# Kernel optimization log

Hardware: AMD Instinct MI355X
Metric: run time of the kernel (lower is better)

The kernel has to match this reference:

```python
import jax, jax.numpy as jnp
import numpy as np

T, B, C, HF, H, W, E, TOP_K = 4, 32, 384, 1536, 14, 14, 8, 2
AUX_W = 0.01
ALPHA = 2.0  # spikingjelly ATan surrogate default

@jax.custom_vjp
def spike(v):
    return (v >= 0.0).astype(v.dtype)

def _spike_fwd(v):
    return spike(v), v

def _spike_bwd(v, g):
    sg = (ALPHA / 2.0) / (1.0 + (jnp.pi / 2.0 * ALPHA * v) ** 2)
    return (g * sg,)

spike.defvjp(_spike_fwd, _spike_bwd)

def lif_multistep(x, tau):
    # x: (T, ...). decay_input=True, v_threshold=1, hard reset to 0, detach_reset
    def step(v, xt):
        v = v + (xt - v) / tau
        s = spike(v - 1.0)
        v = v * (1.0 - jax.lax.stop_gradient(s))
        return v, s
    _, s = jax.lax.scan(step, jnp.zeros_like(x[0]), x)
    return s

def bn_eval(y, gamma, beta, mean, var, eps=1e-5):
    inv = gamma / jnp.sqrt(var + eps)
    return y * inv[None, :, None, None] + (beta - mean * inv)[None, :, None, None]

def setup_inputs() -> dict:
    key = jax.random.key(0)
    ks = jax.random.split(key, 8)
    d = {"x": jax.random.normal(ks[0], (T, B, C, H, W), jnp.float32)}
    d["rw"] = jax.random.normal(ks[1], (E, C), jnp.float32) * 0.02
    d["rb"] = jnp.zeros((E,), jnp.float32)
    d["r_gamma"] = jnp.ones((E,), jnp.float32)
    d["r_beta"] = jnp.zeros((E,), jnp.float32)
    d["r_mean"] = jax.random.normal(ks[2], (E,), jnp.float32) * 0.01
    d["r_var"] = jax.random.uniform(ks[3], (E,), jnp.float32, 0.75, 1.25)
    d["w1"] = jax.random.normal(ks[4], (E, HF, C), jnp.float32) * 0.02
    d["b1"] = jnp.zeros((E, HF), jnp.float32)
    d["g1"] = jnp.ones((E, HF), jnp.float32)
    d["be1"] = jnp.zeros((E, HF), jnp.float32)
    d["m1"] = jax.random.normal(ks[5], (E, HF), jnp.float32) * 0.01
    d["v1"] = jnp.ones((E, HF), jnp.float32)
    d["w2"] = jax.random.normal(ks[6], (E, C, HF), jnp.float32) * 0.02
    d["b2"] = jnp.zeros((E, C), jnp.float32)
    d["g2"] = jnp.ones((E, C), jnp.float32)
    d["be2"] = jnp.zeros((E, C), jnp.float32)
    d["m2"] = jax.random.normal(ks[7], (E, C), jnp.float32) * 0.01
    d["v2"] = jnp.ones((E, C), jnp.float32)
    d["taus"] = jnp.linspace(1.5, 4.0, E, dtype=jnp.float32)
    return d

def reference(x, rw, rb, r_gamma, r_beta, r_mean, r_var,
              w1, b1, g1, be1, m1, v1, w2, b2, g2, be2, m2, v2, taus):
    Tn, Bn, Cn, Hn, Wn = x.shape
    N = Tn * Bn
    # ---- SpikeRouter ----
    s = lif_multistep(x, 2.0)                                   # (T,B,C,H,W)
    r = jnp.einsum('tbchw,ec->tbehw', s, rw) + rb[None, None, :, None, None]
    r = bn_eval(r.reshape(N, E, Hn, Wn), r_gamma, r_beta, r_mean, r_var)
    logits = r.mean(axis=(-2, -1))                              # (N,E)
    probs = jax.nn.softmax(logits, axis=-1)
    tkw, tki = jax.lax.top_k(probs, TOP_K)
    tkw = tkw / tkw.sum(axis=-1, keepdims=True)
    one_hot = jax.nn.one_hot(tki, E, dtype=x.dtype)             # (N,K,E)
    gate = (one_hot * tkw[..., None]).sum(axis=1)               # (N,E), 0 for unselected
    # ---- expert dispatch/combine (dense, math-equivalent: gate==0 masks out) ----
    xt = x.reshape(N, Cn, Hn, Wn)
    out = jnp.zeros_like(xt)
    for e in range(E):
        s1 = spike(xt / taus[e] - 1.0)                          # T=1 LIF step
        h = jnp.einsum('nchw,oc->nohw', s1, w1[e]) + b1[e][None, :, None, None]
        h = bn_eval(h, g1[e], be1[e], m1[e], v1[e])
        s2 = spike(h / taus[e] - 1.0)
        o = jnp.einsum('nchw,oc->nohw', s2, w2[e]) + b2[e][None, :, None, None]
        o = bn_eval(o, g2[e], be2[e], m2[e], v2[e])
        o = o + xt                                              # final residual
        out = out + gate[:, e, None, None, None] * o
    # ---- Switch-style load balancing loss ----
    f = one_hot.sum(axis=1).mean(axis=0)                        # fraction routed per expert
    p = probs.mean(axis=0)
    aux = AUX_W * E * jnp.sum(f * p)
    return out.reshape(Tn, Bn, Cn, Hn, Wn), aux
```

## Files before the change

kernel.cpp:

```cpp
#include <hip/hip_runtime.h>
#include <hip/hip_bf16.h>
#include <cstdint>
#include <math.h>

#define T_  4
#define B_  32
#define C_  384
#define HF_ 1536
#define HW_ 196
#define E_  8
#define N_  128
#define NROW 1792
#define NGT  50176
#define LCAP 64

#define LIFW (B_ * C_ / 4)
#define TRB  (E_ * 12 * 24)
#define PRB  48
#define COMBB ((N_ * C_ * 49) / 256)

__global__ __launch_bounds__(256) void k_lifprep(
    const float* __restrict__ x, float* __restrict__ cnt,
    unsigned int* __restrict__ levels4,
    const float* __restrict__ w1, __hip_bfloat16* __restrict__ w1t,
    const float* b1, const float* g1, const float* be1,
    const float* m1, const float* v1,
    const float* b2, const float* g2, const float* be2,
    const float* m2, const float* v2,
    const float* taus,
    float* A, float* Bc, float* const2, float* inv2v,
    float* rowmaxp, int* header) {
  __shared__ float tile[64][33];
  int blk = blockIdx.x;
  int tid = threadIdx.x;

  if (blk < LIFW) {
    int lane = tid & 63, wave = tid >> 6;
    int bc = blk * 4 + wave;
    bool act = lane < 49;
    float te[E_];
    #pragma unroll
    for (int e2 = 0; e2 < E_; ++e2) {
      float t = taus[e2];
      float y = t;
      #pragma unroll
      for (int it = 0; it < 4; ++it) {
        float cnd = __uint_as_float(__float_as_uint(y) - 1u);
        if (cnd / t - 1.0f >= 0.0f) y = cnd; else break;
      }
      te[e2] = y;
    }
    const float4* xr = (const float4*)x;
    size_t rb = (size_t)bc * 49 + (act ? lane : 0);
    const size_t ts4 = (size_t)B_ * C_ * 49;
    float4 v = {0.f, 0.f, 0.f, 0.f};
    unsigned int counts = 0;
    unsigned int pk[T_];
    #pragma unroll
    for (int t = 0; t < T_; ++t) {
      float4 xv;
      if (act) xv = xr[rb + (size_t)t * ts4];
      else { xv.x = xv.y = xv.z = xv.w = -1e30f; }
      int l0 = 0, l1 = 0, l2 = 0, l3 = 0;
      #pragma unroll
      for (int e2 = 0; e2 < E_; ++e2) {
        l0 += (xv.x >= te[e2]) ? 1 : 0;
        l1 += (xv.y >= te[e2]) ? 1 : 0;
        l2 += (xv.z >= te[e2]) ? 1 : 0;
        l3 += (xv.w >= te[e2]) ? 1 : 0;
      }
      pk[t] = (unsigned int)l0 | ((unsigned int)l1 << 8) |
              ((unsigned int)l2 << 16) | ((unsigned int)l3 << 24);
      v.x = v.x + (xv.x - v.x) * 0.5f;
      v.y = v.y + (xv.y - v.y) * 0.5f;
      v.z = v.z + (xv.z - v.z) * 0.5f;
      v.w = v.w + (xv.w - v.w) * 0.5f;
      int cl = 0;
      if (v.x - 1.0f >= 0.0f) { v.x = 0.f; ++cl; }
      if (v.y - 1.0f >= 0.0f) { v.y = 0.f; ++cl; }
      if (v.z - 1.0f >= 0.0f) { v.z = 0.f; ++cl; }
      if (v.w - 1.0f >= 0.0f) { v.w = 0.f; ++cl; }
      counts += (unsigned int)cl << (8 * t);
    }
    if (act) {
      #pragma unroll
      for (int t = 0; t < T_; ++t)
        levels4[rb + (size_t)t * ts4] = pk[t];
    }
    #pragma unroll
    for (int off = 1; off < 64; off <<= 1)
      counts += (unsigned int)__shfl_xor((int)counts, off, 64);
    if (lane == 0) {
      #pragma unroll
      for (int t = 0; t < T_; ++t)
        cnt[(size_t)t * B_ * C_ + bc] = (float)((counts >> (8 * t)) & 0xffu);
    }
  } else if (blk < LIFW + TRB) {
    int rem = blk - LIFW;
    int e = rem / 288, r2 = rem % 288;
    int ct = r2 / 24, ot = r2 % 24;
    int c0 = ct * 32, o0 = ot * 64;
    int cl = tid & 31, olb = tid >> 5;
    #pragma unroll
    for (int it = 0; it < 8; ++it) {
      int ol = olb + it * 8;
      tile[ol][cl] = w1[(size_t)(e * HF_ + o0 + ol) * C_ + c0 + cl];
    }
    __syncthreads();
    int ol2 = tid & 63, clb = tid >> 6;
    #pragma unroll
    for (int it = 0; it < 8; ++it) {
      int cl2 = clb + it * 4;
      w1t[(size_t)(e * C_ + c0 + cl2) * HF_ + o0 + ol2] =
          __float2bfloat16(tile[ol2][cl2]);
    }
    if (tid < 32) {
      float m = 0.f;
      for (int ol = 0; ol < 64; ++ol) {
        float bv = __bfloat162float(__float2bfloat16(tile[ol][tid]));
        m = fmaxf(m, fabsf(bv));
      }
      rowmaxp[(size_t)(e * C_ + c0 + tid) * 24 + ot] = m;
    }
  } else {
    int idx = (blk - LIFW - TRB) * 256 + tid;
    if (idx < 64) header[idx] = 0;
    if (idx < E_ * HF_) {
      int e = idx / HF_;
      float inv = g1[idx] / sqrtf(v1[idx] + 1e-5f);
      float sh  = be1[idx] - m1[idx] * inv;
      A[idx]  = inv;
      Bc[idx] = inv * b1[idx] + sh - taus[e];
    }
    if (idx < E_ * C_) {
      float inv = g2[idx] / sqrtf(v2[idx] + 1e-5f);
      const2[idx] = b2[idx] * inv + (be2[idx] - m2[idx] * inv);
      inv2v[idx]  = inv;
    }
  }
}

__global__ __launch_bounds__(256) void k_router(
    const float* __restrict__ cnt, const float* __restrict__ rw,
    const float* rb, const float* rg, const float* rbeta,
    const float* rmean, const float* rvar,
    const float* __restrict__ const2,
    const float* __restrict__ rowmaxp, float* __restrict__ rowmax,
    const float* __restrict__ A, const float* __restrict__ Bc,
    float* __restrict__ thrmin,
    int* sel_e, float* sel_g, float* gsum, float* K,
    float* f_acc, float* p_acc) {
  __shared__ float sc[C_ + 256 + E_];
  __shared__ int s_i1, s_i2;
  __shared__ float s_g1, s_g2;
  int bid = blockIdx.x, tid = threadIdx.x;

  if (bid < N_) {
    int n = bid;
    float* part = sc + C_;
    float* lg = part + 256;
    for (int c = tid; c < C_; c += 256) sc[c] = cnt[(size_t)n * C_ + c];
    __syncthreads();
    {
      int e = tid >> 5, sub = tid & 31;
      float d = 0.f;
      for (int c = sub; c < C_; c += 32) d += rw[e * C_ + c] * sc[c];
      part[tid] = d;
    }
    __syncthreads();
    if (tid < E_) {
      float dot = 0.f;
      #pragma unroll
      for (int j = 0; j < 32; ++j) dot += part[tid * 32 + j];
      float inv = rg[tid] / sqrtf(rvar[tid] + 1e-5f);
      lg[tid] = (dot * (1.0f / HW_) + rb[tid]) * inv +
                (rbeta[tid] - rmean[tid] * inv);
    }
    __syncthreads();
    if (tid == 0) {
      float m = lg[0];
      for (int e = 1; e < E_; ++e) m = fmaxf(m, lg[e]);
      float pr[E_]; float s = 0.f;
      for (int e = 0; e < E_; ++e) { pr[e] = expf(lg[e] - m); s += pr[e]; }
      float invs = 1.0f / s;
      for (int e = 0; e < E_; ++e) pr[e] *= invs;
      int i1 = 0;
      for (int e = 1; e < E_; ++e) if (pr[e] > pr[i1]) i1 = e;
      int i2 = (i1 == 0) ? 1 : 0;
      for (int e = 0; e < E_; ++e) if (e != i1 && pr[e] > pr[i2]) i2 = e;
      float w = pr[i1] + pr[i2];
      float ga = pr[i1] / w, gb = pr[i2] / w;
      sel_e[2 * n] = i1; sel_e[2 * n + 1] = i2;
      sel_g[2 * n] = ga; sel_g[2 * n + 1] = gb;
      gsum[n] = ga + gb;
      s_i1 = i1; s_i2 = i2; s_g1 = ga; s_g2 = gb;
      atomicAdd(&f_acc[i1], 1.0f);
      atomicAdd(&f_acc[i2], 1.0f);
      for (int e = 0; e < E_; ++e) atomicAdd(&p_acc[e], pr[e]);
    }
    __syncthreads();
    int i1 = s_i1, i2 = s_i2; float ga = s_g1, gb = s_g2;
    for (int c = tid; c < C_; c += 256)
      K[(size_t)n * C_ + c] =
          ga * const2[i1 * C_ + c] + gb * const2[i2 * C_ + c];
  } else if (bid < N_ + 12) {
    int idx = (bid - N_) * 256 + tid;
    if (idx < E_ * C_) {
      float m = 0.f;
      #pragma unroll
      for (int t = 0; t < 24; ++t) m = fmaxf(m, rowmaxp[(size_t)idx * 24 + t]);
      rowmax[idx] = m;
    }
  } else {
    float* red = sc;
    for (int e = 0; e < E_; ++e) {
      float m = INFINITY;
      for (int o = tid; o < HF_; o += 256) {
        float a = A[e * HF_ + o], b = Bc[e * HF_ + o];
        float thr = (a != 0.0f) ? (-b / fabsf(a))
                                : ((b >= 0.0f) ? -INFINITY : INFINITY);
        m = fminf(m, thr);
      }
      red[tid] = m;
      __syncthreads();
      for (int s = 128; s > 0; s >>= 1) {
        if (tid < s) red[tid] = fminf(red[tid], red[tid + s]);
        __syncthreads();
      }
      if (tid == 0) thrmin[e] = red[0];
      __syncthreads();
    }
  }
}

__global__ __launch_bounds__(256) void k_lists(
    const float* __restrict__ x, const unsigned char* __restrict__ levels,
    const int* __restrict__ sel_e,
    const float* __restrict__ rowmax, const float* __restrict__ thrmin,
    unsigned short* __restrict__ list16,
    int* __restrict__ queue, int* __restrict__ qcount,
    const float* __restrict__ f_acc, const float* __restrict__ p_acc,
    float* __restrict__ aux_out,
    const float* __restrict__ gsum, const float* __restrict__ K,
    float* __restrict__ out) {
  __shared__ unsigned char xs8[14 * C_];
  int bid = blockIdx.x, tid = threadIdx.x;

  if (bid >= NROW) {
    int idx = (bid - NROW) * 256 + tid;
    int nc = idx / 49;
    float g = gsum[nc / C_];
    float kc = K[nc];
    float4 v = ((const float4*)x)[idx];
    v.x = g * v.x + kc;
    v.y = g * v.y + kc;
    v.z = g * v.z + kc;
    v.w = g * v.w + kc;
    ((float4*)out)[idx] = v;
    return;
  }

  int lane = tid & 63, wave = tid >> 6;
  int n = bid / 14, h = bid - n * 14;
  unsigned long long lmask = (1ull << lane) - 1ull;

  if (bid == 0 && tid == 0) {
    float s = 0.f;
    for (int e = 0; e < E_; ++e)
      s += (f_acc[e] * (1.0f / N_)) * (p_acc[e] * (1.0f / N_));
    *aux_out = 0.01f * E_ * s;
  }

  for (int c = tid; c < C_; c += 256) {
    const unsigned short* p =
        (const unsigned short*)(levels + (size_t)(n * C_ + c) * HW_ + h * 14);
    #pragma unroll
    for (int i = 0; i < 7; ++i) {
      unsigned short u = p[i];
      xs8[(2 * i) * C_ + c]     = (unsigned char)(u & 0xff);
      xs8[(2 * i + 1) * C_ + c] = (unsigned char)(u >> 8);
    }
  }
  __syncthreads();

  for (int t = wave; t < 28; t += 4) {
    int k = t / 14, w = t - k * 14;
    int pair = 2 * n + k;
    int e = sel_e[pair];
    const float* rme = rowmax + e * C_;
    unsigned long long masks[6];
    int nnz = 0;
    float myb = 0.f;
    #pragma unroll
    for (int cb = 0; cb < 6; ++cb) {
      int c = cb * 64 + lane;
      bool sp = ((int)xs8[w * C_ + c] > e);
      unsigned long long m = __ballot(sp);
      masks[cb] = m;
      if (sp) myb += rme[c];
      nnz += __popcll(m);
    }
    #pragma unroll
    for (int off = 1; off < 64; off <<= 1) myb += __shfl_xor(myb, off, 64);
    bool prune = (myb < thrmin[e] - 1e-4f);
    if (!prune) {
      int tw = pair * 196 + h * 14 + w;
      size_t lbase = (size_t)tw * LCAP;
      int cum = 0;
      #pragma unroll
      for (int cb = 0; cb < 6; ++cb) {
        unsigned long long m = masks[cb];
        bool sp = (m >> lane) & 1ull;
        int pos = cum + __popcll(m & lmask);
        if (sp && pos < LCAP) list16[lbase + pos] = (unsigned short)(cb * 64 + lane);
        cum += __popcll(m);
      }
      if (lane == 0) {
        int nv = nnz < LCAP ? nnz : LCAP;
        int qi = atomicAdd(qcount, 1);
        queue[qi] = tw | (nv << 20);
      }
    }
  }
}

__global__ __launch_bounds__(256, 4) void k_gather(
    const __hip_bfloat16* __restrict__ w1t,
    const float* __restrict__ A, const float* __restrict__ Bc,
    const int* __restrict__ sel_e, const float* __restrict__ sel_g,
    const int* __restrict__ queue, const int* __restrict__ qcount,
    const unsigned short* __restrict__ list16,
    const float* __restrict__ inv2v, const float* __restrict__ w2,
    float* __restrict__ out) {
  int nq = *qcount;
  int wid = blockIdx.x * 4 + (threadIdx.x >> 6);
  int lane = threadIdx.x & 63;
  int nwaves = gridDim.x * 4;

  for (int qi = wid; qi < nq; qi += nwaves) {
    int ent = queue[qi];
    int tw = ent & 0xFFFFF;
    int nnz = ent >> 20;
    int pair = tw / HW_, pos = tw - pair * HW_;
    int n = pair >> 1;
    int e = sel_e[pair];
    int lv = (int)list16[(size_t)tw * LCAP + lane];
    const uint4* wb = (const uint4*)(w1t + (size_t)e * C_ * HF_);

    #pragma unroll
    for (int pass = 0; pass < 3; ++pass) {
      const uint4* wbp = wb + pass * 64 + lane;
      float acc[8];
      #pragma unroll
      for (int q = 0; q < 8; ++q) acc[q] = 0.f;
      int j = 0;
      for (; j + 4 <= nnz; j += 4) {
        int c0 = __shfl(lv, j + 0);
        int c1 = __shfl(lv, j + 1);
        int c2 = __shfl(lv, j + 2);
        int c3 = __shfl(lv, j + 3);
        uint4 a = wbp[c0 * 192];
        uint4 b = wbp[c1 * 192];
        uint4 c = wbp[c2 * 192];
        uint4 d = wbp[c3 * 192];
        uint32_t ua[4] = {a.x, a.y, a.z, a.w};
        uint32_t ub[4] = {b.x, b.y, b.z, b.w};
        uint32_t uc[4] = {c.x, c.y, c.z, c.w};
        uint32_t ud[4] = {d.x, d.y, d.z, d.w};
        #pragma unroll
        for (int q = 0; q < 4; ++q) {
          acc[2 * q]     += __uint_as_float(ua[q] << 16) + __uint_as_float(ub[q] << 16) +
                            __uint_as_float(uc[q] << 16) + __uint_as_float(ud[q] << 16);
          acc[2 * q + 1] += __uint_as_float(ua[q] & 0xffff0000u) + __uint_as_float(ub[q] & 0xffff0000u) +
                            __uint_as_float(uc[q] & 0xffff0000u) + __uint_as_float(ud[q] & 0xffff0000u);
        }
      }
      for (; j < nnz; ++j) {
        int c0 = __shfl(lv, j);
        uint4 a = wbp[c0 * 192];
        uint32_t ua[4] = {a.x, a.y, a.z, a.w};
        #pragma unroll
        for (int q = 0; q < 4; ++q) {
          acc[2 * q]     += __uint_as_float(ua[q] << 16);
          acc[2 * q + 1] += __uint_as_float(ua[q] & 0xffff0000u);
        }
      }
      int k2 = (pass * 64 + lane) * 2;
      float4 Av0 = ((const float4*)(A + e * HF_))[k2];
      float4 Av1 = ((const float4*)(A + e * HF_))[k2 + 1];
      float4 Bv0 = ((const float4*)(Bc + e * HF_))[k2];
      float4 Bv1 = ((const float4*)(Bc + e * HF_))[k2 + 1];
      float av[8] = {Av0.x, Av0.y, Av0.z, Av0.w, Av1.x, Av1.y, Av1.z, Av1.w};
      float bv[8] = {Bv0.x, Bv0.y, Bv0.z, Bv0.w, Bv1.x, Bv1.y, Bv1.z, Bv1.w};
      #pragma unroll
      for (int q = 0; q < 8; ++q) {
        unsigned long long fm = __ballot(av[q] * acc[q] + bv[q] >= 0.0f);
        while (fm) {
          int b = __ffsll((unsigned long long)fm) - 1;
          fm &= fm - 1;
          int o = (pass * 64 + b) * 8 + q;
          float gk = sel_g[pair];
          const float* w2r = w2 + (size_t)e * C_ * HF_ + o;
          const float* ivr = inv2v + e * C_;
          for (int c = lane; c < C_; c += 64) {
            atomicAdd(&out[((size_t)(n * C_ + c)) * HW_ + pos],
                      gk * ivr[c] * w2r[(size_t)c * HF_]);
          }
        }
      }
    }
  }
}

extern "C" void kernel_launch(void* const* d_in, const int* in_sizes, int n_in,
                              void* d_out, int out_size, void* d_ws, size_t ws_size,
                              hipStream_t stream) {
  const float* x       = (const float*)d_in[0];
  const float* rw      = (const float*)d_in[1];
  const float* rb      = (const float*)d_in[2];
  const float* r_gamma = (const float*)d_in[3];
  const float* r_beta  = (const float*)d_in[4];
  const float* r_mean  = (const float*)d_in[5];
  const float* r_var   = (const float*)d_in[6];
  const float* w1      = (const float*)d_in[7];
  const float* b1      = (const float*)d_in[8];
  const float* g1      = (const float*)d_in[9];
  const float* be1     = (const float*)d_in[10];
  const float* m1      = (const float*)d_in[11];
  const float* v1      = (const float*)d_in[12];
  const float* w2      = (const float*)d_in[13];
  const float* b2      = (const float*)d_in[14];
  const float* g2      = (const float*)d_in[15];
  const float* be2     = (const float*)d_in[16];
  const float* m2      = (const float*)d_in[17];
  const float* v2      = (const float*)d_in[18];
  const float* taus    = (const float*)d_in[19];
  float* out = (float*)d_out;

  char* ws = (char*)d_ws;
  int*   header = (int*)ws;
  float* f_acc  = (float*)ws + 8;
  float* p_acc  = (float*)ws + 16;
  float* cnt    = (float*)(ws + 256);
  int*   sel_e  = (int*)(ws + 196864);
  float* sel_g  = (float*)(ws + 197888);
  float* gsum   = (float*)(ws + 198912);
  float* K      = (float*)(ws + 199424);
  float* A      = (float*)(ws + 396032);
  float* Bc     = (float*)(ws + 445184);
  float* const2 = (float*)(ws + 494336);
  float* inv2v  = (float*)(ws + 506624);
  __hip_bfloat16* w1t = (__hip_bfloat16*)(ws + 715520);
  int*   queue  = (int*)(ws + 10152704);
  unsigned short* list16 = (unsigned short*)(ws + 10353408);
  float* rowmaxp = (float*)(ws + 16775936);
  float* rowmax  = (float*)(ws + 17070848);
  float* thrmin  = (float*)(ws + 17083136);
  unsigned char* levels = (unsigned char*)(ws + 17084416);
  int* qcount = header + 1;

  k_lifprep<<<LIFW + TRB + PRB, 256, 0, stream>>>(
      x, cnt, (unsigned int*)levels, w1, w1t,
      b1, g1, be1, m1, v1, b2, g2, be2, m2, v2, taus,
      A, Bc, const2, inv2v, rowmaxp, header);
  k_router<<<N_ + 13, 256, 0, stream>>>(
      cnt, rw, rb, r_gamma, r_beta, r_mean, r_var, const2,
      rowmaxp, rowmax, A, Bc, thrmin,
      sel_e, sel_g, gsum, K, f_acc, p_acc);
  k_lists<<<NROW + COMBB, 256, 0, stream>>>(
      x, levels, sel_e, rowmax, thrmin, list16, queue, qcount,
      f_acc, p_acc, out + (out_size - 1), gsum, K, out);
  k_gather<<<2048, 256, 0, stream>>>(
      w1t, A, Bc, sel_e, sel_g, queue, qcount, list16, inv2v, w2, out);
}
```

Measured before the change: 201.4 us.

## Prune hidden-unit groups in gather via per-group weight-max upper bounds

```diff
diff --git a/kernel.cpp b/kernel.cpp
--- a/kernel.cpp
+++ b/kernel.cpp
@@ -13,6 +13,7 @@
 #define NROW 1792
 #define NGT  50176
 #define LCAP 64
+#define NGRP 24
 
 #define LIFW (B_ * C_ / 4)
 #define TRB  (E_ * 12 * 24)
@@ -120,7 +121,7 @@
         float bv = __bfloat162float(__float2bfloat16(tile[ol][tid]));
         m = fmaxf(m, fabsf(bv));
       }
-      rowmaxp[(size_t)(e * C_ + c0 + tid) * 24 + ot] = m;
+      rowmaxp[(size_t)(e * C_ + c0 + tid) * NGRP + ot] = m;
     }
   } else {
     int idx = (blk - LIFW - TRB) * 256 + tid;
@@ -147,7 +148,7 @@
     const float* __restrict__ const2,
     const float* __restrict__ rowmaxp, float* __restrict__ rowmax,
     const float* __restrict__ A, const float* __restrict__ Bc,
-    float* __restrict__ thrmin,
+    float* __restrict__ thrmin, float* __restrict__ thrg,
     int* sel_e, float* sel_g, float* gsum, float* K,
     float* f_acc, float* p_acc) {
   __shared__ float sc[C_ + 256 + E_];
@@ -208,27 +209,29 @@
     if (idx < E_ * C_) {
       float m = 0.f;
       #pragma unroll
-      for (int t = 0; t < 24; ++t) m = fmaxf(m, rowmaxp[(size_t)idx * 24 + t]);
+      for (int t = 0; t < NGRP; ++t)
+        m = fmaxf(m, rowmaxp[(size_t)idx * NGRP + t]);
       rowmax[idx] = m;
     }
   } else {
-    float* red = sc;
+    int lane = tid & 63, wv = tid >> 6;
     for (int e = 0; e < E_; ++e) {
-      float m = INFINITY;
-      for (int o = tid; o < HF_; o += 256) {
+      for (int g = wv; g < NGRP; g += 4) {
+        int o = g * 64 + lane;
         float a = A[e * HF_ + o], b = Bc[e * HF_ + o];
         float thr = (a != 0.0f) ? (-b / fabsf(a))
                                 : ((b >= 0.0f) ? -INFINITY : INFINITY);
-        m = fminf(m, thr);
-      }
-      red[tid] = m;
-      __syncthreads();
-      for (int s = 128; s > 0; s >>= 1) {
-        if (tid < s) red[tid] = fminf(red[tid], red[tid + s]);
-        __syncthreads();
-      }
-      if (tid == 0) thrmin[e] = red[0];
-      __syncthreads();
+        #pragma unroll
+        for (int off = 1; off < 64; off <<= 1)
+          thr = fminf(thr, __shfl_xor(thr, off, 64));
+        if (lane == 0) thrg[e * NGRP + g] = thr;
+      }
+    }
+    __syncthreads();
+    if (tid < E_) {
+      float m = INFINITY;
+      for (int g = 0; g < NGRP; ++g) m = fminf(m, thrg[tid * NGRP + g]);
+      thrmin[tid] = m;
     }
   }
 }
@@ -330,6 +333,7 @@
     const int* __restrict__ sel_e, const float* __restrict__ sel_g,
     const int* __restrict__ queue, const int* __restrict__ qcount,
     const unsigned short* __restrict__ list16,
+    const float* __restrict__ grpmax, const float* __restrict__ thrg,
     const float* __restrict__ inv2v, const float* __restrict__ w2,
     float* __restrict__ out) {
   int nq = *qcount;
@@ -345,67 +349,61 @@
     int n = pair >> 1;
     int e = sel_e[pair];
     int lv = (int)list16[(size_t)tw * LCAP + lane];
-    const uint4* wb = (const uint4*)(w1t + (size_t)e * C_ * HF_);
-
-    #pragma unroll
-    for (int pass = 0; pass < 3; ++pass) {
-      const uint4* wbp = wb + pass * 64 + lane;
-      float acc[8];
-      #pragma unroll
-      for (int q = 0; q < 8; ++q) acc[q] = 0.f;
-      int j = 0;
-      for (; j + 4 <= nnz; j += 4) {
-        int c0 = __shfl(lv, j + 0);
-        int c1 = __shfl(lv, j + 1);
-        int c2 = __shfl(lv, j + 2);
-        int c3 = __shfl(lv, j + 3);
-        uint4 a = wbp[c0 * 192];
-        uint4 b = wbp[c1 * 192];
-        uint4 c = wbp[c2 * 192];
-        uint4 d = wbp[c3 * 192];
-        uint32_t ua[4] = {a.x, a.y, a.z, a.w};
-        uint32_t ub[4] = {b.x, b.y, b.z, b.w};
-        uint32_t uc[4] = {c.x, c.y, c.z, c.w};
-        uint32_t ud[4] = {d.x, d.y, d.z, d.w};
-        #pragma unroll
-        for (int q = 0; q < 4; ++q) {
-          acc[2 * q]     += __uint_as_float(ua[q] << 16) + __uint_as_float(ub[q] << 16) +
-                            __uint_as_float(uc[q] << 16) + __uint_as_float(ud[q] << 16);
-          acc[2 * q + 1] += __uint_as_float(ua[q] & 0xffff0000u) + __uint_as_float(ub[q] & 0xffff0000u) +
-                            __uint_as_float(uc[q] & 0xffff0000u) + __uint_as_float(ud[q] & 0xffff0000u);
-        }
-      }
-      for (; j < nnz; ++j) {
-        int c0 = __shfl(lv, j);
-        uint4 a = wbp[c0 * 192];
-        uint32_t ua[4] = {a.x, a.y, a.z, a.w};
-        #pragma unroll
-        for (int q = 0; q < 4; ++q) {
-          acc[2 * q]     += __uint_as_float(ua[q] << 16);
-          acc[2 * q + 1] += __uint_as_float(ua[q] & 0xffff0000u);
-        }
-      }
-      int k2 = (pass * 64 + lane) * 2;
-      float4 Av0 = ((const float4*)(A + e * HF_))[k2];
-      float4 Av1 = ((const float4*)(A + e * HF_))[k2 + 1];
-      float4 Bv0 = ((const float4*)(Bc + e * HF_))[k2];
-      float4 Bv1 = ((const float4*)(Bc + e * HF_))[k2 + 1];
-      float av[8] = {Av0.x, Av0.y, Av0.z, Av0.w, Av1.x, Av1.y, Av1.z, Av1.w};
-      float bv[8] = {Bv0.x, Bv0.y, Bv0.z, Bv0.w, Bv1.x, Bv1.y, Bv1.z, Bv1.w};
-      #pragma unroll
-      for (int q = 0; q < 8; ++q) {
-        unsigned long long fm = __ballot(av[q] * acc[q] + bv[q] >= 0.0f);
-        while (fm) {
-          int b = __ffsll((unsigned long long)fm) - 1;
-          fm &= fm - 1;
-          int o = (pass * 64 + b) * 8 + q;
-          float gk = sel_g[pair];
-          const float* w2r = w2 + (size_t)e * C_ * HF_ + o;
-          const float* ivr = inv2v + e * C_;
-          for (int c = lane; c < C_; c += 64) {
-            atomicAdd(&out[((size_t)(n * C_ + c)) * HW_ + pos],
-                      gk * ivr[c] * w2r[(size_t)c * HF_]);
-          }
+
+    bool actg = lane < NGRP;
+    int gl = actg ? lane : 0;
+    const float* gme = grpmax + (size_t)e * C_ * NGRP;
+    float myb = 0.f;
+    int j = 0;
+    for (; j + 4 <= nnz; j += 4) {
+      int c0 = __shfl(lv, j + 0), c1 = __shfl(lv, j + 1);
+      int c2 = __shfl(lv, j + 2), c3 = __shfl(lv, j + 3);
+      float a0 = gme[(size_t)c0 * NGRP + gl];
+      float a1 = gme[(size_t)c1 * NGRP + gl];
+      float a2 = gme[(size_t)c2 * NGRP + gl];
+      float a3 = gme[(size_t)c3 * NGRP + gl];
+      myb += (a0 + a1) + (a2 + a3);
+    }
+    for (; j < nnz; ++j) {
+      int c0 = __shfl(lv, j);
+      myb += gme[(size_t)c0 * NGRP + gl];
+    }
+    unsigned long long gmask =
+        __ballot(actg && (myb >= thrg[e * NGRP + gl] - 1e-4f));
+
+    while (gmask) {
+      int g = __ffsll(gmask) - 1;
+      gmask &= gmask - 1;
+      int o = g * 64 + lane;
+      const unsigned short* wcol =
+          (const unsigned short*)w1t + (size_t)e * C_ * HF_ + o;
+      float acc = 0.f;
+      int j2 = 0;
+      for (; j2 + 4 <= nnz; j2 += 4) {
+        int c0 = __shfl(lv, j2 + 0), c1 = __shfl(lv, j2 + 1);
+        int c2 = __shfl(lv, j2 + 2), c3 = __shfl(lv, j2 + 3);
+        float b0 = __uint_as_float((unsigned)wcol[(size_t)c0 * HF_] << 16);
+        float b1 = __uint_as_float((unsigned)wcol[(size_t)c1 * HF_] << 16);
+        float b2 = __uint_as_float((unsigned)wcol[(size_t)c2 * HF_] << 16);
+        float b3 = __uint_as_float((unsigned)wcol[(size_t)c3 * HF_] << 16);
+        acc += (b0 + b1) + (b2 + b3);
+      }
+      for (; j2 < nnz; ++j2) {
+        int c0 = __shfl(lv, j2);
+        acc += __uint_as_float((unsigned)wcol[(size_t)c0 * HF_] << 16);
+      }
+      float av = A[e * HF_ + o], bv = Bc[e * HF_ + o];
+      unsigned long long fm = __ballot(av * acc + bv >= 0.0f);
+      while (fm) {
+        int b = __ffsll(fm) - 1;
+        fm &= fm - 1;
+        int oo = g * 64 + b;
+        float gk = sel_g[pair];
+        const float* w2r = w2 + (size_t)e * C_ * HF_ + oo;
+        const float* ivr = inv2v + e * C_;
+        for (int c = lane; c < C_; c += 64) {
+          atomicAdd(&out[((size_t)(n * C_ + c)) * HW_ + pos],
+                    gk * ivr[c] * w2r[(size_t)c * HF_]);
         }
       }
     }
@@ -456,6 +454,7 @@
   float* rowmaxp = (float*)(ws + 16775936);
   float* rowmax  = (float*)(ws + 17070848);
   float* thrmin  = (float*)(ws + 17083136);
+  float* thrg    = (float*)(ws + 17083200);
   unsigned char* levels = (unsigned char*)(ws + 17084416);
   int* qcount = header + 1;
 
@@ -465,11 +464,12 @@
       A, Bc, const2, inv2v, rowmaxp, header);
   k_router<<<N_ + 13, 256, 0, stream>>>(
       cnt, rw, rb, r_gamma, r_beta, r_mean, r_var, const2,
-      rowmaxp, rowmax, A, Bc, thrmin,
+      rowmaxp, rowmax, A, Bc, thrmin, thrg,
       sel_e, sel_g, gsum, K, f_acc, p_acc);
   k_lists<<<NROW + COMBB, 256, 0, stream>>>(
       x, levels, sel_e, rowmax, thrmin, list16, queue, qcount,
       f_acc, p_acc, out + (out_size - 1), gsum, K, out);
   k_gather<<<2048, 256, 0, stream>>>(
-      w1t, A, Bc, sel_e, sel_g, queue, qcount, list16, inv2v, w2, out);
+      w1t, A, Bc, sel_e, sel_g, queue, qcount, list16,
+      rowmaxp, thrg, inv2v, w2, out);
 }
```

New measurement: 207.6 us. 3.1% more time.

## Bucket gather queue per expert and fuse three accumulation passes into one

Applied to the files above, without the earlier changes.

```diff
diff --git a/kernel.cpp b/kernel.cpp
--- a/kernel.cpp
+++ b/kernel.cpp
@@ -13,6 +13,7 @@
 #define NROW 1792
 #define NGT  50176
 #define LCAP 64
+#define NGRP 24
 
 #define LIFW (B_ * C_ / 4)
 #define TRB  (E_ * 12 * 24)
@@ -120,7 +121,7 @@
         float bv = __bfloat162float(__float2bfloat16(tile[ol][tid]));
         m = fmaxf(m, fabsf(bv));
       }
-      rowmaxp[(size_t)(e * C_ + c0 + tid) * 24 + ot] = m;
+      rowmaxp[(size_t)(e * C_ + c0 + tid) * NGRP + ot] = m;
     }
   } else {
     int idx = (blk - LIFW - TRB) * 256 + tid;
@@ -208,7 +209,8 @@
     if (idx < E_ * C_) {
       float m = 0.f;
       #pragma unroll
-      for (int t = 0; t < 24; ++t) m = fmaxf(m, rowmaxp[(size_t)idx * 24 + t]);
+      for (int t = 0; t < NGRP; ++t)
+        m = fmaxf(m, rowmaxp[(size_t)idx * NGRP + t]);
       rowmax[idx] = m;
     }
   } else {
@@ -317,8 +319,8 @@
       }
       if (lane == 0) {
         int nv = nnz < LCAP ? nnz : LCAP;
-        int qi = atomicAdd(qcount, 1);
-        queue[qi] = tw | (nv << 20);
+        int qi = atomicAdd(&qcount[e], 1);
+        queue[e * NGT + qi] = tw | (nv << 20);
       }
     }
   }
@@ -327,65 +329,78 @@
 __global__ __launch_bounds__(256, 4) void k_gather(
     const __hip_bfloat16* __restrict__ w1t,
     const float* __restrict__ A, const float* __restrict__ Bc,
-    const int* __restrict__ sel_e, const float* __restrict__ sel_g,
+    const float* __restrict__ sel_g,
     const int* __restrict__ queue, const int* __restrict__ qcount,
     const unsigned short* __restrict__ list16,
     const float* __restrict__ inv2v, const float* __restrict__ w2,
     float* __restrict__ out) {
-  int nq = *qcount;
+  int cum[E_ + 1];
+  cum[0] = 0;
+  #pragma unroll
+  for (int e2 = 0; e2 < E_; ++e2) cum[e2 + 1] = cum[e2] + qcount[e2];
+  int nq = cum[E_];
   int wid = blockIdx.x * 4 + (threadIdx.x >> 6);
   int lane = threadIdx.x & 63;
   int nwaves = gridDim.x * 4;
-
-  for (int qi = wid; qi < nq; qi += nwaves) {
-    int ent = queue[qi];
+  int chunk = (nq + nwaves - 1) / nwaves;
+  int start = wid * chunk;
+  int end = start + chunk; if (end > nq) end = nq;
+
+  for (int gidx = start; gidx < end; ++gidx) {
+    int e = 0;
+    #pragma unroll
+    for (int k = 1; k < E_; ++k) e += (gidx >= cum[k]) ? 1 : 0;
+    int ent = queue[e * NGT + (gidx - cum[e])];
     int tw = ent & 0xFFFFF;
     int nnz = ent >> 20;
     int pair = tw / HW_, pos = tw - pair * HW_;
     int n = pair >> 1;
-    int e = sel_e[pair];
     int lv = (int)list16[(size_t)tw * LCAP + lane];
     const uint4* wb = (const uint4*)(w1t + (size_t)e * C_ * HF_);
-
-    #pragma unroll
-    for (int pass = 0; pass < 3; ++pass) {
-      const uint4* wbp = wb + pass * 64 + lane;
-      float acc[8];
-      #pragma unroll
-      for (int q = 0; q < 8; ++q) acc[q] = 0.f;
-      int j = 0;
-      for (; j + 4 <= nnz; j += 4) {
-        int c0 = __shfl(lv, j + 0);
-        int c1 = __shfl(lv, j + 1);
-        int c2 = __shfl(lv, j + 2);
-        int c3 = __shfl(lv, j + 3);
-        uint4 a = wbp[c0 * 192];
-        uint4 b = wbp[c1 * 192];
-        uint4 c = wbp[c2 * 192];
-        uint4 d = wbp[c3 * 192];
-        uint32_t ua[4] = {a.x, a.y, a.z, a.w};
-        uint32_t ub[4] = {b.x, b.y, b.z, b.w};
-        uint32_t uc[4] = {c.x, c.y, c.z, c.w};
-        uint32_t ud[4] = {d.x, d.y, d.z, d.w};
-        #pragma unroll
-        for (int q = 0; q < 4; ++q) {
-          acc[2 * q]     += __uint_as_float(ua[q] << 16) + __uint_as_float(ub[q] << 16) +
-                            __uint_as_float(uc[q] << 16) + __uint_as_float(ud[q] << 16);
-          acc[2 * q + 1] += __uint_as_float(ua[q] & 0xffff0000u) + __uint_as_float(ub[q] & 0xffff0000u) +
-                            __uint_as_float(uc[q] & 0xffff0000u) + __uint_as_float(ud[q] & 0xffff0000u);
-        }
-      }
-      for (; j < nnz; ++j) {
-        int c0 = __shfl(lv, j);
-        uint4 a = wbp[c0 * 192];
-        uint32_t ua[4] = {a.x, a.y, a.z, a.w};
-        #pragma unroll
-        for (int q = 0; q < 4; ++q) {
-          acc[2 * q]     += __uint_as_float(ua[q] << 16);
-          acc[2 * q + 1] += __uint_as_float(ua[q] & 0xffff0000u);
-        }
-      }
-      int k2 = (pass * 64 + lane) * 2;
+    const uint4* wbp0 = wb + lane;
+    const uint4* wbp1 = wb + 64 + lane;
+    const uint4* wbp2 = wb + 128 + lane;
+
+    float acc[24];
+    #pragma unroll
+    for (int q = 0; q < 24; ++q) acc[q] = 0.f;
+    int j = 0;
+    for (; j + 2 <= nnz; j += 2) {
+      int c0 = __shfl(lv, j), c1 = __shfl(lv, j + 1);
+      uint4 a0 = wbp0[c0 * 192];
+      uint4 a1 = wbp1[c0 * 192];
+      uint4 a2 = wbp2[c0 * 192];
+      uint4 b0 = wbp0[c1 * 192];
+      uint4 b1 = wbp1[c1 * 192];
+      uint4 b2 = wbp2[c1 * 192];
+      uint32_t uu[12] = {a0.x, a0.y, a0.z, a0.w, a1.x, a1.y, a1.z, a1.w,
+                         a2.x, a2.y, a2.z, a2.w};
+      uint32_t vv[12] = {b0.x, b0.y, b0.z, b0.w, b1.x, b1.y, b1.z, b1.w,
+                         b2.x, b2.y, b2.z, b2.w};
+      #pragma unroll
+      for (int q = 0; q < 12; ++q) {
+        acc[2 * q]     += __uint_as_float(uu[q] << 16) +
+                          __uint_as_float(vv[q] << 16);
+        acc[2 * q + 1] += __uint_as_float(uu[q] & 0xffff0000u) +
+                          __uint_as_float(vv[q] & 0xffff0000u);
+      }
+    }
+    for (; j < nnz; ++j) {
+      int c0 = __shfl(lv, j);
+      uint4 a0 = wbp0[c0 * 192];
+      uint4 a1 = wbp1[c0 * 192];
+      uint4 a2 = wbp2[c0 * 192];
+      uint32_t uu[12] = {a0.x, a0.y, a0.z, a0.w, a1.x, a1.y, a1.z, a1.w,
+                         a2.x, a2.y, a2.z, a2.w};
+      #pragma unroll
+      for (int q = 0; q < 12; ++q) {
+        acc[2 * q]     += __uint_as_float(uu[q] << 16);
+        acc[2 * q + 1] += __uint_as_float(uu[q] & 0xffff0000u);
+      }
+    }
+    #pragma unroll
+    for (int p = 0; p < 3; ++p) {
+      int k2 = (p * 64 + lane) * 2;
       float4 Av0 = ((const float4*)(A + e * HF_))[k2];
       float4 Av1 = ((const float4*)(A + e * HF_))[k2 + 1];
       float4 Bv0 = ((const float4*)(Bc + e * HF_))[k2];
@@ -394,13 +409,13 @@
       float bv[8] = {Bv0.x, Bv0.y, Bv0.z, Bv0.w, Bv1.x, Bv1.y, Bv1.z, Bv1.w};
       #pragma unroll
       for (int q = 0; q < 8; ++q) {
-        unsigned long long fm = __ballot(av[q] * acc[q] + bv[q] >= 0.0f);
+        unsigned long long fm = __ballot(av[q] * acc[p * 8 + q] + bv[q] >= 0.0f);
         while (fm) {
-          int b = __ffsll((unsigned long long)fm) - 1;
+          int b = __ffsll(fm) - 1;
           fm &= fm - 1;
-          int o = (pass * 64 + b) * 8 + q;
+          int oo = (p * 64 + b) * 8 + q;
           float gk = sel_g[pair];
-          const float* w2r = w2 + (size_t)e * C_ * HF_ + o;
+          const float* w2r = w2 + (size_t)e * C_ * HF_ + oo;
           const float* ivr = inv2v + e * C_;
           for (int c = lane; c < C_; c += 64) {
             atomicAdd(&out[((size_t)(n * C_ + c)) * HW_ + pos],
@@ -441,6 +456,7 @@
   int*   header = (int*)ws;
   float* f_acc  = (float*)ws + 8;
   float* p_acc  = (float*)ws + 16;
+  int*   qcount = header + 24;
   float* cnt    = (float*)(ws + 256);
   int*   sel_e  = (int*)(ws + 196864);
   float* sel_g  = (float*)(ws + 197888);
@@ -451,13 +467,12 @@
   float* const2 = (float*)(ws + 494336);
   float* inv2v  = (float*)(ws + 506624);
   __hip_bfloat16* w1t = (__hip_bfloat16*)(ws + 715520);
-  int*   queue  = (int*)(ws + 10152704);
   unsigned short* list16 = (unsigned short*)(ws + 10353408);
   float* rowmaxp = (float*)(ws + 16775936);
   float* rowmax  = (float*)(ws + 17070848);
   float* thrmin  = (float*)(ws + 17083136);
   unsigned char* levels = (unsigned char*)(ws + 17084416);
-  int* qcount = header + 1;
+  int*   queue  = (int*)(ws + 26718208);
 
   k_lifprep<<<LIFW + TRB + PRB, 256, 0, stream>>>(
       x, cnt, (unsigned int*)levels, w1, w1t,
@@ -471,5 +486,5 @@
       x, levels, sel_e, rowmax, thrmin, list16, queue, qcount,
       f_acc, p_acc, out + (out_size - 1), gsum, K, out);
   k_gather<<<2048, 256, 0, stream>>>(
-      w1t, A, Bc, sel_e, sel_g, queue, qcount, list16, inv2v, w2, out);
+      w1t, A, Bc, sel_g, queue, qcount, list16, inv2v, w2, out);
 }
```

Measured after the change: 202.9 us. Within noise of the previous version (+0.8%).
